# Optimization experiments

Measured on AMD Instinct MI355X. Metric: run time of the kernel, lower is better.

## Reference

```python
import jax, jax.numpy as jnp
import numpy as np

NUM_HEADS = 16
HIDDEN = 1152
MLP = 4304
HEAD_DIM = HIDDEN // NUM_HEADS  # 72
SEQ = 3072
LN_EPS = 1e-5


def setup_inputs() -> dict:
    key = jax.random.key(0)
    ks = jax.random.split(key, 16)
    inv = 1.0 / np.sqrt(HIDDEN)
    inv_m = 1.0 / np.sqrt(MLP)
    pos = jnp.arange(SEQ, dtype=jnp.float32)[:, None]
    freq = jnp.exp(-jnp.arange(HEAD_DIM // 2, dtype=jnp.float32) * (np.log(10000.0) / (HEAD_DIM // 2)))
    ang = pos * freq[None, :]
    return {
        "hidden_states": jax.random.normal(ks[0], (SEQ, HIDDEN), jnp.float32),
        "rope_cos": jnp.cos(ang),
        "rope_sin": jnp.sin(ang),
        "ln0_g": jnp.ones((HIDDEN,), jnp.float32),
        "ln0_b": jnp.zeros((HIDDEN,), jnp.float32),
        "ln1_g": jnp.ones((HIDDEN,), jnp.float32),
        "ln1_b": jnp.zeros((HIDDEN,), jnp.float32),
        "wqkv_w": jax.random.normal(ks[1], (3 * HIDDEN, HIDDEN), jnp.float32) * inv,
        "wqkv_b": jnp.zeros((3 * HIDDEN,), jnp.float32),
        "wo_w": jax.random.normal(ks[2], (HIDDEN, HIDDEN), jnp.float32) * inv,
        "wo_b": jnp.zeros((HIDDEN,), jnp.float32),
        "fc0_w": jax.random.normal(ks[3], (MLP, HIDDEN), jnp.float32) * inv,
        "fc0_b": jnp.zeros((MLP,), jnp.float32),
        "fc1_w": jax.random.normal(ks[4], (HIDDEN, MLP), jnp.float32) * inv_m,
        "fc1_b": jnp.zeros((HIDDEN,), jnp.float32),
    }


def _layernorm(x, g, b):
    mu = jnp.mean(x, axis=-1, keepdims=True)
    var = jnp.mean(jnp.square(x - mu), axis=-1, keepdims=True)
    return (x - mu) * jax.lax.rsqrt(var + LN_EPS) * g + b


def _apply_rope(x, cos, sin):
    # x: [S, H, Dh]; cos/sin: [S, Dh/2]
    xp = x.astype(jnp.float32).reshape(*x.shape[:-1], -1, 2)  # [S, H, Dh/2, 2]
    xr, xi = xp[..., 0], xp[..., 1]
    c = cos[:, None, :]
    s = sin[:, None, :]
    out_r = xr * c - xi * s
    out_i = xr * s + xi * c
    return jnp.stack([out_r, out_i], axis=-1).reshape(x.shape).astype(x.dtype)


def reference(hidden_states, rope_cos, rope_sin, ln0_g, ln0_b, ln1_g, ln1_b,
              wqkv_w, wqkv_b, wo_w, wo_b, fc0_w, fc0_b, fc1_w, fc1_b):
    S = hidden_states.shape[0]
    residual = hidden_states
    h = _layernorm(hidden_states, ln0_g, ln0_b)
    xqkv = (h @ wqkv_w.T + wqkv_b).reshape(S, 3, NUM_HEADS, HEAD_DIM)
    xq, xk, xv = xqkv[:, 0], xqkv[:, 1], xqkv[:, 2]
    xq = _apply_rope(xq, rope_cos, rope_sin)
    xk = _apply_rope(xk, rope_cos, rope_sin)
    scale = 1.0 / np.sqrt(HEAD_DIM)
    scores = jnp.einsum('shd,thd->hst', xq, xk) * scale  # [H, S, S]
    attn = jax.nn.softmax(scores.astype(jnp.float32), axis=-1).astype(xq.dtype)
    out = jnp.einsum('hst,thd->shd', attn, xv).reshape(S, HIDDEN)
    h = residual + (out @ wo_w.T + wo_b)
    residual = h
    h = _layernorm(h, ln1_g, ln1_b)
    h = jax.nn.gelu(h @ fc0_w.T + fc0_b, approximate=True)
    h = h @ fc1_w.T + fc1_b
    return residual + h
```

## Files before the change

### kernel.cpp

```cpp
#include <hip/hip_runtime.h>
#include <hip/hip_bf16.h>
#include <math.h>

typedef __hip_bfloat16 bf16;
typedef __attribute__((ext_vector_type(8))) short short8;
typedef __attribute__((ext_vector_type(4))) short short4v;
typedef __attribute__((ext_vector_type(4))) float f32x4;

#define SEQ 3072
#define HID 1152
#define NHEAD 16
#define HD 72
#define HDP 96
#define MLPD 4304
#define MLPP 4352

__device__ __forceinline__ void async_lds16(void* lds, const void* g) {
  __builtin_amdgcn_global_load_lds((const __attribute__((address_space(1))) void*)g,
                                   (__attribute__((address_space(3))) void*)lds,
                                   16, 0, 0);
}

__device__ __forceinline__ short bf16b(float x) {
  __hip_bfloat16 h = __float2bfloat16(x);
  return *reinterpret_cast<short*>(&h);
}

__device__ __forceinline__ unsigned cvt_pk2(float a, float b) {
  unsigned r;
  asm("v_cvt_pk_bf16_f32 %0, %1, %2" : "=v"(r) : "v"(a), "v"(b));
  return r;
}

__global__ __launch_bounds__(256) void cast_bf16_k(const float* __restrict__ in,
                                                   unsigned* __restrict__ out2, int n4) {
  int stride = gridDim.x * blockDim.x;
  for (int i = blockIdx.x * blockDim.x + threadIdx.x; i < n4; i += stride) {
    float4 u = ((const float4*)in)[i];
    uint2 w = make_uint2(cvt_pk2(u.x, u.y), cvt_pk2(u.z, u.w));
    ((uint2*)out2)[i] = w;
  }
}

__global__ __launch_bounds__(256) void cast_pad_rows_k(const float* __restrict__ in,
                                                       unsigned* __restrict__ out2,
                                                       int R, int C4, int n4) {
  int stride = gridDim.x * blockDim.x;
  for (int i = blockIdx.x * blockDim.x + threadIdx.x; i < n4; i += stride) {
    int r = i / C4;
    uint2 w = make_uint2(0u, 0u);
    if (r < R) {
      float4 u = ((const float4*)in)[i];
      w = make_uint2(cvt_pk2(u.x, u.y), cvt_pk2(u.z, u.w));
    }
    ((uint2*)out2)[i] = w;
  }
}

__global__ __launch_bounds__(256) void cast_pad_cols_k(const float* __restrict__ in,
                                                       unsigned* __restrict__ out2,
                                                       int C4, int Cp4, int n4) {
  int stride = gridDim.x * blockDim.x;
  for (int i = blockIdx.x * blockDim.x + threadIdx.x; i < n4; i += stride) {
    int r = i / Cp4, c4 = i - r * Cp4;
    uint2 w = make_uint2(0u, 0u);
    if (c4 < C4) {
      float4 u = ((const float4*)in)[r * C4 + c4];
      w = make_uint2(cvt_pk2(u.x, u.y), cvt_pk2(u.z, u.w));
    }
    ((uint2*)out2)[i] = w;
  }
}

__global__ __launch_bounds__(256) void ln_k(const float* __restrict__ x,
                                            const float* __restrict__ g,
                                            const float* __restrict__ b,
                                            bf16* __restrict__ o) {
  int row = blockIdx.x;
  const float4* xr = (const float4*)(x + (size_t)row * HID);
  float sum = 0.f, sq = 0.f;
  for (int c = threadIdx.x; c < HID / 4; c += 256) {
    float4 u = xr[c];
    sum += u.x + u.y + u.z + u.w;
    sq += u.x * u.x + u.y * u.y + u.z * u.z + u.w * u.w;
  }
#pragma unroll
  for (int off = 32; off > 0; off >>= 1) {
    sum += __shfl_down(sum, off, 64);
    sq += __shfl_down(sq, off, 64);
  }
  __shared__ float red[8];
  int wv = threadIdx.x >> 6;
  if ((threadIdx.x & 63) == 0) { red[wv] = sum; red[4 + wv] = sq; }
  __syncthreads();
  if (threadIdx.x == 0) {
    red[0] = red[0] + red[1] + red[2] + red[3];
    red[4] = red[4] + red[5] + red[6] + red[7];
  }
  __syncthreads();
  float mu = red[0] * (1.f / HID);
  float var = red[4] * (1.f / HID) - mu * mu;
  float inv = rsqrtf(var + 1e-5f);
  uint2* o4 = (uint2*)(o + (size_t)row * HID);
  const float4* g4 = (const float4*)g;
  const float4* b4 = (const float4*)b;
  for (int c = threadIdx.x; c < HID / 4; c += 256) {
    float4 u = xr[c], gg = g4[c], bb = b4[c];
    uint2 w = make_uint2(cvt_pk2((u.x - mu) * inv * gg.x + bb.x, (u.y - mu) * inv * gg.y + bb.y),
                         cvt_pk2((u.z - mu) * inv * gg.z + bb.z, (u.w - mu) * inv * gg.w + bb.w));
    o4[c] = w;
  }
}

template <int EPI>
__global__ __launch_bounds__(256) void gemm_bf16(const bf16* __restrict__ A,
                                                 const bf16* __restrict__ Bt,
                                                 const float* __restrict__ bias, int nbias,
                                                 const float* __restrict__ res,
                                                 float* __restrict__ outf,
                                                 bf16* __restrict__ outb,
                                                 int M, int N, int K) {
  __shared__ bf16 As[3][128 * 32];
  __shared__ bf16 Bs[3][128 * 32];
  const int t = threadIdx.x;
  const int l = t & 63;
  const int w = t >> 6;
  const int wr = w >> 1, wc = w & 1;
  const int lrow = l & 15;
  const int lk = (l >> 4) * 8;
  const int m0 = blockIdx.y * 128;
  const int n0 = blockIdx.x * 128;
  const int arow = t >> 2;
  const int ach = (t & 3) * 8;

  const bf16* pa0 = &A[(size_t)(m0 + arow) * K + ach];
  const bf16* pa1 = &A[(size_t)(m0 + arow + 64) * K + ach];
  const bf16* pb0 = &Bt[(size_t)(n0 + arow) * K + ach];
  const bf16* pb1 = &Bt[(size_t)(n0 + arow + 64) * K + ach];
  auto STAGE = [&](int buf, int kt) {
    size_t off = (size_t)kt * 32;
    async_lds16(&As[buf][t * 8], pa0 + off);
    async_lds16(&As[buf][(256 + t) * 8], pa1 + off);
    async_lds16(&Bs[buf][t * 8], pb0 + off);
    async_lds16(&Bs[buf][(256 + t) * 8], pb1 + off);
  };

  f32x4 acc[4][4] = {};
  const int nkt = K >> 5;
  STAGE(0, 0);
  STAGE(1, 1);
  int bcur = 0;
  for (int kt = 0; kt < nkt; ++kt) {
    if (kt + 1 < nkt) {
      asm volatile("s_waitcnt vmcnt(4)" ::: "memory");
    } else {
      asm volatile("s_waitcnt vmcnt(0)" ::: "memory");
    }
    __builtin_amdgcn_s_barrier();
    int bn2 = bcur + 2;
    if (bn2 >= 3) bn2 -= 3;
    if (kt + 2 < nkt) STAGE(bn2, kt + 2);

    short8 af[4], bfr[4];
#pragma unroll
    for (int i = 0; i < 4; ++i)
      af[i] = *(const short8*)&As[bcur][(wr * 64 + i * 16 + lrow) * 32 + lk];
#pragma unroll
    for (int i = 0; i < 4; ++i)
      bfr[i] = *(const short8*)&Bs[bcur][(wc * 64 + i * 16 + lrow) * 32 + lk];
    __builtin_amdgcn_s_setprio(1);
#pragma unroll
    for (int i = 0; i < 4; ++i)
#pragma unroll
      for (int j = 0; j < 4; ++j)
        acc[i][j] = __builtin_amdgcn_mfma_f32_16x16x32_bf16(af[i], bfr[j], acc[i][j], 0, 0, 0);
    __builtin_amdgcn_s_setprio(0);
    ++bcur;
    if (bcur == 3) bcur = 0;
  }

#pragma unroll
  for (int i = 0; i < 4; ++i) {
    int rowb = m0 + wr * 64 + i * 16 + (l >> 4) * 4;
#pragma unroll
    for (int j = 0; j < 4; ++j) {
      int col = n0 + wc * 64 + j * 16 + lrow;
      float bv = (col < nbias) ? bias[col] : 0.f;
#pragma unroll
      for (int r2 = 0; r2 < 4; ++r2) {
        size_t idx = (size_t)(rowb + r2) * N + col;
        float v = acc[i][j][r2] + bv;
        if (EPI == 0) {
          outf[idx] = v;
        } else if (EPI == 1) {
          outf[idx] = v + res[idx];
        } else {
          float gel = 0.5f * v * (1.f + tanhf(0.7978845608028654f * (v + 0.044715f * v * v * v)));
          outb[idx] = __float2bfloat16(gel);
        }
      }
    }
  }
}

__global__ __launch_bounds__(256) void rope_split(const float* __restrict__ xqkv,
                                                  const float* __restrict__ cosb,
                                                  const float* __restrict__ sinb,
                                                  bf16* __restrict__ qp,
                                                  bf16* __restrict__ kp,
                                                  bf16* __restrict__ vt) {
  __shared__ bf16 vl[64][72];
  const int t = threadIdx.x;
  const int h = blockIdx.y;
  const int s0 = blockIdx.x * 64;
  const float scale = 0.11785113019775793f;
  for (int idx = t; idx < 64 * 48; idx += 256) {
    int sl = idx / 48, pi = idx - sl * 48;
    int srow = s0 + sl;
    size_t obase = ((size_t)h * SEQ + srow) * HDP + 2 * pi;
    if (pi < 36) {
      const float* xr = xqkv + (size_t)srow * (3 * HID) + h * HD + 2 * pi;
      float qr = xr[0], qi = xr[1];
      float kr = xr[HID], ki = xr[HID + 1];
      float c = cosb[srow * 36 + pi], sn = sinb[srow * 36 + pi];
      *(unsigned*)&qp[obase] = cvt_pk2((qr * c - qi * sn) * scale, (qr * sn + qi * c) * scale);
      *(unsigned*)&kp[obase] = cvt_pk2(kr * c - ki * sn, kr * sn + ki * c);
    } else {
      *(unsigned*)&qp[obase] = 0u;
      *(unsigned*)&kp[obase] = 0u;
    }
  }
  for (int idx = t; idx < 64 * 72; idx += 256) {
    int sl = idx / 72, d = idx - sl * 72;
    vl[sl][d] = __float2bfloat16(xqkv[(size_t)(s0 + sl) * (3 * HID) + 2 * HID + h * HD + d]);
  }
  __syncthreads();
  bf16 z = __float2bfloat16(0.f);
  for (int idx = t; idx < HDP * 64; idx += 256) {
    int d = idx / 64, sl = idx - d * 64;
    vt[((size_t)h * HDP + d) * SEQ + s0 + sl] = (d < 72) ? vl[sl][d] : z;
  }
}

__global__ __launch_bounds__(256) void flash_attn(const bf16* __restrict__ q,
                                                  const bf16* __restrict__ kk,
                                                  const bf16* __restrict__ vT,
                                                  bf16* __restrict__ o) {
  __shared__ alignas(16) bf16 KV3[3 * 6144];
  __shared__ alignas(16) bf16 Pl[4][512];
  const int t = threadIdx.x;
  const int l = t & 63;
  const int w = t >> 6;
  const int g = l >> 4;
  const int lrow = l & 15;
  const int bid = blockIdx.x;
  const int kq = bid >> 3;
  const int h = (bid & 7) * 2 + (kq & 1);
  const int q0 = (kq >> 1) * 64 + w * 16;
  const int NT = SEQ / 32;

  const bf16* sbase[3];
  int smul[3];
#pragma unroll
  for (int i = 0; i < 3; ++i) {
    int s = t + i * 256;
    if (s < 384) {
      int cb = s >> 5, kv = s & 31;
      sbase[i] = kk + ((size_t)h * SEQ + kv) * HDP + cb * 8;
      smul[i] = 32 * HDP;
    } else {
      int vs = s - 384;
      int cb = vs / 96, d = vs - cb * 96;
      sbase[i] = vT + ((size_t)h * HDP + d) * SEQ + cb * 8;
      smul[i] = 32;
    }
  }
  auto STAGE = [&](int tile, int bufOff) {
#pragma unroll
    for (int i = 0; i < 3; ++i)
      async_lds16(&KV3[bufOff + (t + i * 256) * 8], sbase[i] + (size_t)tile * smul[i]);
  };

  short8 qf[3];
#pragma unroll
  for (int f = 0; f < 3; ++f)
    qf[f] = *(const short8*)&q[((size_t)h * SEQ + q0 + lrow) * HDP + f * 32 + g * 8];

  float m_r = -1e30f, l_r = 0.f;
  f32x4 oa[5] = {};

  STAGE(0, 0);
  STAGE(1, 6144);
  STAGE(2, 12288);
  asm volatile("s_waitcnt vmcnt(6)" ::: "memory");
  __builtin_amdgcn_s_barrier();

  f32x4 stA[2] = {}, stB[2];
  int b0 = 0;
#pragma unroll
  for (int nf = 0; nf < 2; ++nf)
#pragma unroll
    for (int f = 0; f < 3; ++f) {
      short8 kfrag = *(const short8*)&KV3[0 + (f * 4 + g) * 256 + (nf * 16 + lrow) * 8];
      stA[nf] = __builtin_amdgcn_mfma_f32_16x16x32_bf16(kfrag, qf[f], stA[nf], 0, 0, 0);
    }

  for (int kt = 0; kt < NT - 1; ++kt) {
    int b1 = b0 + 6144;
    if (b1 == 18432) b1 = 0;
    asm volatile("s_waitcnt vmcnt(3)" ::: "memory");
    __builtin_amdgcn_s_barrier();

    stB[0] = (f32x4){0.f, 0.f, 0.f, 0.f};
    stB[1] = (f32x4){0.f, 0.f, 0.f, 0.f};
    __builtin_amdgcn_s_setprio(1);
#pragma unroll
    for (int nf = 0; nf < 2; ++nf)
#pragma unroll
      for (int f = 0; f < 3; ++f) {
        short8 kfrag = *(const short8*)&KV3[b1 + (f * 4 + g) * 256 + (nf * 16 + lrow) * 8];
        stB[nf] = __builtin_amdgcn_mfma_f32_16x16x32_bf16(kfrag, qf[f], stB[nf], 0, 0, 0);
      }
    __builtin_amdgcn_s_setprio(0);

    float pmax = fmaxf(fmaxf(fmaxf(stA[0][0], stA[0][1]), fmaxf(stA[0][2], stA[0][3])),
                       fmaxf(fmaxf(stA[1][0], stA[1][1]), fmaxf(stA[1][2], stA[1][3])));
    if (!__all(pmax - m_r <= 8.f)) {
      float rm = pmax;
      rm = fmaxf(rm, __shfl_xor(rm, 16, 64));
      rm = fmaxf(rm, __shfl_xor(rm, 32, 64));
      float mn = fmaxf(m_r, rm);
      float alpha = __expf(m_r - mn);
      l_r *= alpha;
#pragma unroll
      for (int nf = 0; nf < 5; ++nf)
#pragma unroll
        for (int r = 0; r < 4; ++r) oa[nf][r] *= alpha;
      m_r = mn;
    }
#pragma unroll
    for (int nf = 0; nf < 2; ++nf)
#pragma unroll
      for (int r = 0; r < 4; ++r) stA[nf][r] = __expf(stA[nf][r] - m_r);
    l_r += (stA[0][0] + stA[0][1]) + (stA[0][2] + stA[0][3]) +
           (stA[1][0] + stA[1][1]) + (stA[1][2] + stA[1][3]);

#pragma unroll
    for (int nf = 0; nf < 2; ++nf) {
      uint2* dst = (uint2*)&Pl[w][(2 * nf + (g >> 1)) * 128 + lrow * 8 + (g & 1) * 4];
      *dst = make_uint2(cvt_pk2(stA[nf][0], stA[nf][1]), cvt_pk2(stA[nf][2], stA[nf][3]));
    }

    {
      short8 pa = *(const short8*)&Pl[w][g * 128 + lrow * 8];
      __builtin_amdgcn_s_setprio(1);
#pragma unroll
      for (int nf = 0; nf < 5; ++nf) {
        short8 bv = *(const short8*)&KV3[b0 + 3072 + g * 768 + (nf * 16 + lrow) * 8];
        oa[nf] = __builtin_amdgcn_mfma_f32_16x16x32_bf16(bv, pa, oa[nf], 0, 0, 0);
      }
      __builtin_amdgcn_s_setprio(0);
    }

    asm volatile("s_waitcnt lgkmcnt(0)" ::: "memory");
    __builtin_amdgcn_s_barrier();
    int s = kt + 3;
    if (s >= NT) s -= NT;
    STAGE(s, b0);
    stA[0] = stB[0];
    stA[1] = stB[1];
    b0 = b1;
  }

  {
    float pmax = fmaxf(fmaxf(fmaxf(stA[0][0], stA[0][1]), fmaxf(stA[0][2], stA[0][3])),
                       fmaxf(fmaxf(stA[1][0], stA[1][1]), fmaxf(stA[1][2], stA[1][3])));
    if (!__all(pmax - m_r <= 8.f)) {
      float rm = pmax;
      rm = fmaxf(rm, __shfl_xor(rm, 16, 64));
      rm = fmaxf(rm, __shfl_xor(rm, 32, 64));
      float mn = fmaxf(m_r, rm);
      float alpha = __expf(m_r - mn);
      l_r *= alpha;
#pragma unroll
      for (int nf = 0; nf < 5; ++nf)
#pragma unroll
        for (int r = 0; r < 4; ++r) oa[nf][r] *= alpha;
      m_r = mn;
    }
#pragma unroll
    for (int nf = 0; nf < 2; ++nf)
#pragma unroll
      for (int r = 0; r < 4; ++r) stA[nf][r] = __expf(stA[nf][r] - m_r);
    l_r += (stA[0][0] + stA[0][1]) + (stA[0][2] + stA[0][3]) +
           (stA[1][0] + stA[1][1]) + (stA[1][2] + stA[1][3]);
#pragma unroll
    for (int nf = 0; nf < 2; ++nf) {
      uint2* dst = (uint2*)&Pl[w][(2 * nf + (g >> 1)) * 128 + lrow * 8 + (g & 1) * 4];
      *dst = make_uint2(cvt_pk2(stA[nf][0], stA[nf][1]), cvt_pk2(stA[nf][2], stA[nf][3]));
    }
    short8 pa = *(const short8*)&Pl[w][g * 128 + lrow * 8];
#pragma unroll
    for (int nf = 0; nf < 5; ++nf) {
      short8 bv = *(const short8*)&KV3[b0 + 3072 + g * 768 + (nf * 16 + lrow) * 8];
      oa[nf] = __builtin_amdgcn_mfma_f32_16x16x32_bf16(bv, pa, oa[nf], 0, 0, 0);
    }
  }

  float lt = l_r;
  lt += __shfl_xor(lt, 16, 64);
  lt += __shfl_xor(lt, 32, 64);
  float rcp = 1.f / lt;
  size_t obase = (size_t)(q0 + lrow) * HID + h * HD;
#pragma unroll
  for (int nf = 0; nf < 5; ++nf) {
    int d = nf * 16 + g * 4;
    if (d + 3 < HD) {
      uint2 pk = make_uint2(cvt_pk2(oa[nf][0] * rcp, oa[nf][1] * rcp),
                            cvt_pk2(oa[nf][2] * rcp, oa[nf][3] * rcp));
      *(uint2*)&o[obase + d] = pk;
    }
  }
}

extern "C" void kernel_launch(void* const* d_in, const int* in_sizes, int n_in,
                              void* d_out, int out_size, void* d_ws, size_t ws_size,
                              hipStream_t stream) {
  (void)in_sizes; (void)n_in; (void)out_size;
  const float* hidden = (const float*)d_in[0];
  const float* cosb = (const float*)d_in[1];
  const float* sinb = (const float*)d_in[2];
  const float* ln0g = (const float*)d_in[3];
  const float* ln0b = (const float*)d_in[4];
  const float* ln1g = (const float*)d_in[5];
  const float* ln1b = (const float*)d_in[6];
  const float* wqkv = (const float*)d_in[7];
  const float* bqkv = (const float*)d_in[8];
  const float* wo = (const float*)d_in[9];
  const float* bo = (const float*)d_in[10];
  const float* w0 = (const float*)d_in[11];
  const float* b0 = (const float*)d_in[12];
  const float* w1 = (const float*)d_in[13];
  const float* b1 = (const float*)d_in[14];

  char* p = (char*)d_ws;
  auto alloc = [&](size_t n) {
    char* r = p;
    p += (n + 255) & ~(size_t)255;
    return r;
  };
  bf16* wqkv_bf = (bf16*)alloc((size_t)3 * HID * HID * 2);
  bf16* wo_bf = (bf16*)alloc((size_t)HID * HID * 2);
  bf16* fc0_bf = (bf16*)alloc((size_t)MLPP * HID * 2);
  bf16* fc1_bf = (bf16*)alloc((size_t)HID * MLPP * 2);
  bf16* ln0_bf = (bf16*)alloc((size_t)SEQ * HID * 2);
  float* xqkv = (float*)alloc((size_t)SEQ * 3 * HID * 4);
  bf16* qp = (bf16*)alloc((size_t)NHEAD * SEQ * HDP * 2);
  bf16* kp = (bf16*)alloc((size_t)NHEAD * SEQ * HDP * 2);
  bf16* vt = (bf16*)alloc((size_t)NHEAD * HDP * SEQ * 2);
  bf16* attn_bf = (bf16*)alloc((size_t)SEQ * HID * 2);
  float* h1 = (float*)alloc((size_t)SEQ * HID * 4);
  bf16* ln1_bf = (bf16*)alloc((size_t)SEQ * HID * 2);
  bf16* gelu_bf = (bf16*)alloc((size_t)SEQ * MLPP * 2);
  if ((size_t)(p - (char*)d_ws) > ws_size) return;

  dim3 blk(256);
  cast_bf16_k<<<2048, blk, 0, stream>>>(wqkv, (unsigned*)wqkv_bf, 3 * HID * HID / 4);
  cast_bf16_k<<<1024, blk, 0, stream>>>(wo, (unsigned*)wo_bf, HID * HID / 4);
  cast_pad_rows_k<<<2048, blk, 0, stream>>>(w0, (unsigned*)fc0_bf, MLPD, HID / 4, MLPP * HID / 4);
  cast_pad_cols_k<<<2048, blk, 0, stream>>>(w1, (unsigned*)fc1_bf, MLPD / 4, MLPP / 4, HID * MLPP / 4);
  ln_k<<<SEQ, blk, 0, stream>>>(hidden, ln0g, ln0b, ln0_bf);
  gemm_bf16<0><<<dim3(3 * HID / 128, SEQ / 128), blk, 0, stream>>>(
      ln0_bf, wqkv_bf, bqkv, 3 * HID, nullptr, xqkv, nullptr, SEQ, 3 * HID, HID);
  rope_split<<<dim3(SEQ / 64, NHEAD), blk, 0, stream>>>(xqkv, cosb, sinb, qp, kp, vt);
  flash_attn<<<dim3(768), blk, 0, stream>>>(qp, kp, vt, attn_bf);
  gemm_bf16<1><<<dim3(HID / 128, SEQ / 128), blk, 0, stream>>>(
      attn_bf, wo_bf, bo, HID, hidden, h1, nullptr, SEQ, HID, HID);
  ln_k<<<SEQ, blk, 0, stream>>>(h1, ln1g, ln1b, ln1_bf);
  gemm_bf16<2><<<dim3(MLPP / 128, SEQ / 128), blk, 0, stream>>>(
      ln1_bf, fc0_bf, b0, MLPD, nullptr, nullptr, gelu_bf, SEQ, MLPP, HID);
  gemm_bf16<1><<<dim3(HID / 128, SEQ / 128), blk, 0, stream>>>(
      gelu_bf, fc1_bf, b1, HID, h1, (float*)d_out, nullptr, SEQ, HID, MLPP);
}
```

Measured before the change: 401.1 us.

## Deepen GEMM pipeline to four stages, remap blocks XCD-aware, cheaper GELU

The GEMM now keeps four LDS stages with three tiles in flight instead of two, which aims to hide more global-load latency. It also uses a 1D grid whose block index is remapped so that consecutive blocks on the same XCD cover neighbouring tiles, improving L2 reuse. The tanh-based GELU is replaced by a clamped exp formulation. The extra stage raises LDS use, which may reduce occupancy, and the pipeline now issues redundant wraparound loads on its last iterations.

```diff
diff --git a/kernel.cpp b/kernel.cpp
--- a/kernel.cpp
+++ b/kernel.cpp
@@ -120,16 +120,21 @@
                                                  float* __restrict__ outf,
                                                  bf16* __restrict__ outb,
                                                  int M, int N, int K) {
-  __shared__ bf16 As[3][128 * 32];
-  __shared__ bf16 Bs[3][128 * 32];
+  __shared__ bf16 As[4][128 * 32];
+  __shared__ bf16 Bs[4][128 * 32];
   const int t = threadIdx.x;
   const int l = t & 63;
   const int w = t >> 6;
   const int wr = w >> 1, wc = w & 1;
   const int lrow = l & 15;
   const int lk = (l >> 4) * 8;
-  const int m0 = blockIdx.y * 128;
-  const int n0 = blockIdx.x * 128;
+  const int total = gridDim.x;
+  const int wg = (blockIdx.x & 7) * (total >> 3) + (blockIdx.x >> 3);
+  const int gyt = M >> 7;
+  const int xt = wg / gyt;
+  const int yt = wg - xt * gyt;
+  const int m0 = yt * 128;
+  const int n0 = xt * 128;
   const int arow = t >> 2;
   const int ach = (t & 3) * 8;
 
@@ -149,18 +154,15 @@
   const int nkt = K >> 5;
   STAGE(0, 0);
   STAGE(1, 1);
-  int bcur = 0;
+  STAGE(2, 2);
   for (int kt = 0; kt < nkt; ++kt) {
-    if (kt + 1 < nkt) {
-      asm volatile("s_waitcnt vmcnt(4)" ::: "memory");
-    } else {
-      asm volatile("s_waitcnt vmcnt(0)" ::: "memory");
-    }
+    asm volatile("s_waitcnt vmcnt(8)" ::: "memory");
     __builtin_amdgcn_s_barrier();
-    int bn2 = bcur + 2;
-    if (bn2 >= 3) bn2 -= 3;
-    if (kt + 2 < nkt) STAGE(bn2, kt + 2);
-
+    int ks = kt + 3;
+    if (ks >= nkt) ks -= nkt;
+    STAGE((kt + 3) & 3, ks);
+
+    const int bcur = kt & 3;
     short8 af[4], bfr[4];
 #pragma unroll
     for (int i = 0; i < 4; ++i)
@@ -175,9 +177,8 @@
       for (int j = 0; j < 4; ++j)
         acc[i][j] = __builtin_amdgcn_mfma_f32_16x16x32_bf16(af[i], bfr[j], acc[i][j], 0, 0, 0);
     __builtin_amdgcn_s_setprio(0);
-    ++bcur;
-    if (bcur == 3) bcur = 0;
-  }
+  }
+  asm volatile("s_waitcnt vmcnt(0)" ::: "memory");
 
 #pragma unroll
   for (int i = 0; i < 4; ++i) {
@@ -195,8 +196,10 @@
         } else if (EPI == 1) {
           outf[idx] = v + res[idx];
         } else {
-          float gel = 0.5f * v * (1.f + tanhf(0.7978845608028654f * (v + 0.044715f * v * v * v)));
-          outb[idx] = __float2bfloat16(gel);
+          float u = 0.7978845608028654f * (v + 0.044715f * v * v * v);
+          u = fminf(fmaxf(u, -15.f), 15.f);
+          float tt = __expf(2.f * u);
+          outb[idx] = __float2bfloat16(v * tt / (tt + 1.f));
         }
       }
     }
@@ -470,15 +473,15 @@
   cast_pad_rows_k<<<2048, blk, 0, stream>>>(w0, (unsigned*)fc0_bf, MLPD, HID / 4, MLPP * HID / 4);
   cast_pad_cols_k<<<2048, blk, 0, stream>>>(w1, (unsigned*)fc1_bf, MLPD / 4, MLPP / 4, HID * MLPP / 4);
   ln_k<<<SEQ, blk, 0, stream>>>(hidden, ln0g, ln0b, ln0_bf);
-  gemm_bf16<0><<<dim3(3 * HID / 128, SEQ / 128), blk, 0, stream>>>(
+  gemm_bf16<0><<<dim3((3 * HID / 128) * (SEQ / 128)), blk, 0, stream>>>(
       ln0_bf, wqkv_bf, bqkv, 3 * HID, nullptr, xqkv, nullptr, SEQ, 3 * HID, HID);
   rope_split<<<dim3(SEQ / 64, NHEAD), blk, 0, stream>>>(xqkv, cosb, sinb, qp, kp, vt);
   flash_attn<<<dim3(768), blk, 0, stream>>>(qp, kp, vt, attn_bf);
-  gemm_bf16<1><<<dim3(HID / 128, SEQ / 128), blk, 0, stream>>>(
+  gemm_bf16<1><<<dim3((HID / 128) * (SEQ / 128)), blk, 0, stream>>>(
       attn_bf, wo_bf, bo, HID, hidden, h1, nullptr, SEQ, HID, HID);
   ln_k<<<SEQ, blk, 0, stream>>>(h1, ln1g, ln1b, ln1_bf);
-  gemm_bf16<2><<<dim3(MLPP / 128, SEQ / 128), blk, 0, stream>>>(
+  gemm_bf16<2><<<dim3((MLPP / 128) * (SEQ / 128)), blk, 0, stream>>>(
       ln1_bf, fc0_bf, b0, MLPD, nullptr, nullptr, gelu_bf, SEQ, MLPP, HID);
-  gemm_bf16<1><<<dim3(HID / 128, SEQ / 128), blk, 0, stream>>>(
+  gemm_bf16<1><<<dim3((HID / 128) * (SEQ / 128)), blk, 0, stream>>>(
       gelu_bf, fc1_bf, b1, HID, h1, (float*)d_out, nullptr, SEQ, HID, MLPP);
 }
```

Result: slower. 410.1 us (+2.2%).
